# Kernel tuning notes

Hardware: AMD Instinct MI355X
Metric: run time of the kernel (lower is better)

The kernel has to match this reference:

```python
import jax, jax.numpy as jnp
import numpy as np

# Problem sizes
N, D, B = 4096, 2048, 64  # nodes, feature dim, sequential samples
# LARFDSSOM hyperparameters (from __init__ defaults)
A_T = 0.3          # activation threshold
DSBETA = 1e-4      # moving-average rate
E_B = 0.5          # winner learning rate
E_N = 0.01 * E_B   # neighbor learning rate (e_n is multiplied by e_b in __init__)
EPS_DS = 0.01      # relevance smoothing


def setup_inputs() -> dict:
    key = jax.random.key(0)
    k0, k1, k2, k3, k4 = jax.random.split(key, 5)
    return {
        "x": jax.random.uniform(k0, (B, D), jnp.float32),
        "weights": jax.random.uniform(k1, (N, D), jnp.float32),
        "moving_avg": jax.random.uniform(k2, (N, D), jnp.float32),
        "relevances": jax.random.uniform(k3, (N, D), jnp.float32),
        "wins": jnp.zeros((N,), jnp.float32),
        "neighbors": jax.random.randint(k4, (N, N), 0, 2) > 0,
    }


def _som_steps(x, weights, moving_avg, relevances, wins, neighbors):
    """Sequential LARFDSSOM update_map over B samples (codebook at max size,
    so the add_node branch is structurally impossible and the per-sample step
    is either 'update winner + neighbors' or a no-op)."""
    node_ids = jnp.arange(weights.shape[0])

    def step(state, w):
        W, M, R, wn = state
        diff = w[None, :] - W                          # [N, D]
        # weighted_distance + activation
        dists = jnp.sum(R * diff * diff, axis=1)       # [N]
        rel_sum = jnp.sum(R, axis=1)                   # [N]
        act = rel_sum / (rel_sum + dists + 1e-7)
        winner = jnp.argmax(act)
        do_upd = act[winner] >= A_T                    # else no-op (codebook full)
        is_winner = node_ids == winner
        is_nb = neighbors[winner] & (~is_winner)
        # per-node learning rate: e_b for winner, e_n for neighbors, 0 otherwise
        lr = jnp.where(is_winner, E_B, jnp.where(is_nb, E_N, 0.0))[:, None]  # [N, 1]
        # update_node (vectorized over all nodes, masked below)
        dist_abs = jnp.abs(diff)
        M_new = lr * DSBETA * dist_abs + (1.0 - lr * DSBETA) * M
        mx = jnp.max(M_new, axis=1, keepdims=True)
        mn = jnp.min(M_new, axis=1, keepdims=True)
        av = jnp.mean(M_new, axis=1, keepdims=True)
        denom = EPS_DS * (mx - mn)
        # denom == 0 -> original produces NaN then sets relevance to 1.0
        arg = jnp.clip((M_new - av) / jnp.where(denom == 0.0, 1.0, denom), -80.0, 80.0)
        R_new = jnp.where(denom == 0.0, 1.0, 1.0 / (1.0 + jnp.exp(arg)))
        W_new = W + lr * diff
        m = (do_upd & (lr[:, 0] > 0.0))[:, None]       # rows actually touched
        W = jnp.where(m, W_new, W)
        M = jnp.where(m, M_new, M)
        R = jnp.where(m, R_new, R)
        wn = wn + jnp.where(is_winner & do_upd, 1.0, 0.0)
        return (W, M, R, wn), None

    (W, M, R, wn), _ = jax.lax.scan(step, (weights, moving_avg, relevances, wins), x)
    return W


def reference(x, weights, moving_avg, relevances, wins, neighbors):
    return _som_steps(x, weights, moving_avg, relevances, wins, neighbors)
```

## Files before the change

kernel.cpp:

```cpp
#include <hip/hip_runtime.h>
#include <cstddef>

#define NN 4096
#define DD 2048
#define BB 64

constexpr float kAT     = 0.3f;
constexpr float kDSBETA = 1e-4f;
constexpr float kEB     = 0.5f;
constexpr float kEN     = 0.005f;
constexpr float kEPS    = 0.01f;

__device__ __forceinline__ float wave_sum_f(float v) {
#pragma unroll
    for (int o = 32; o; o >>= 1) v += __shfl_xor(v, o, 64);
    return v;
}
__device__ __forceinline__ double wave_sum_d(double v) {
#pragma unroll
    for (int o = 32; o; o >>= 1) v += __shfl_xor(v, o, 64);
    return v;
}
__device__ __forceinline__ float wave_max_f(float v) {
#pragma unroll
    for (int o = 32; o; o >>= 1) v = fmaxf(v, __shfl_xor(v, o, 64));
    return v;
}
__device__ __forceinline__ float wave_min_f(float v) {
#pragma unroll
    for (int o = 32; o; o >>= 1) v = fminf(v, __shfl_xor(v, o, 64));
    return v;
}
__device__ __forceinline__ unsigned long long wave_max_u64(unsigned long long v) {
#pragma unroll
    for (int o = 32; o; o >>= 1) {
        const unsigned long long u = __shfl_xor(v, o, 64);
        v = (u > v) ? u : v;
    }
    return v;
}

__global__ void detect_nb(const unsigned char* __restrict__ nb, unsigned* __restrict__ flag) {
    unsigned v = 0;
    const int i0 = threadIdx.x * 256;
    for (int i = 0; i < 256; i++) {
        const int idx = i0 + i;
        if ((idx & 3) != 0) v |= nb[idx];
    }
    if (v != 0) atomicOr(flag, 1u);
}

__global__ __launch_bounds__(256) void som_step(
    const float* __restrict__ x_upd,
    const float* __restrict__ x_act,
    float* __restrict__ W,
    float* __restrict__ M,
    float* __restrict__ R,
    const void* __restrict__ nb,
    const unsigned* __restrict__ flag,
    const unsigned long long* __restrict__ part_upd,
    unsigned long long* __restrict__ part_act,
    const int stride)
{
    const int n   = blockIdx.x;
    const int tid = threadIdx.x;
    __shared__ float  sred[3][4];
    __shared__ double sredd[2][4];

    float lr = 0.0f;
    if (part_upd != nullptr) {
        unsigned long long k = part_upd[(size_t)(tid & 63) * stride];
        k = wave_max_u64(k);
        const double act_w = __longlong_as_double((long long)(k & ~0xFFFULL));
        const int winner   = 4095 - (int)(k & 0xFFFULL);
        if (act_w >= (double)kAT) {
            if (n == winner) {
                lr = kEB;
            } else {
                const size_t off = (size_t)winner * NN + n;
                const bool isnb = (*flag != 0)
                    ? (((const unsigned char*)nb)[off] != 0)
                    : (((const int*)nb)[off] != 0);
                if (isnb) lr = kEN;
            }
        }
    }
    const bool next = (x_act != nullptr);
    if (lr == 0.0f && !next) return;

    const size_t rowoff = (size_t)n * DD + (size_t)tid * 8;
    const size_t xoff   = (size_t)tid * 8;
    float w[8], r[8];
    *(float4*)(w)     = *(const float4*)(W + rowoff);
    *(float4*)(w + 4) = *(const float4*)(W + rowoff + 4);

    if (lr != 0.0f) {
        float m[8], xu[8], mnew[8];
        *(float4*)(m)      = *(const float4*)(M + rowoff);
        *(float4*)(m + 4)  = *(const float4*)(M + rowoff + 4);
        *(float4*)(xu)     = *(const float4*)(x_upd + xoff);
        *(float4*)(xu + 4) = *(const float4*)(x_upd + xoff + 4);

        const float c1 = lr * kDSBETA;
        const float c2 = 1.0f - c1;
        float psum = 0.0f, pmx = -INFINITY, pmn = INFINITY;
#pragma unroll
        for (int j = 0; j < 8; j++) {
            const float d = xu[j] - w[j];
            w[j] = w[j] + lr * d;
            const float mv = c1 * fabsf(d) + c2 * m[j];
            mnew[j] = mv;
            psum += mv;
            pmx = fmaxf(pmx, mv);
            pmn = fminf(pmn, mv);
        }
        psum = wave_sum_f(psum); pmx = wave_max_f(pmx); pmn = wave_min_f(pmn);
        const int wid = tid >> 6, lane = tid & 63;
        if (lane == 0) { sred[0][wid] = psum; sred[1][wid] = pmx; sred[2][wid] = pmn; }
        __syncthreads();
        const float ts  = sred[0][0] + sred[0][1] + sred[0][2] + sred[0][3];
        const float tmx = fmaxf(fmaxf(sred[1][0], sred[1][1]), fmaxf(sred[1][2], sred[1][3]));
        const float tmn = fminf(fminf(sred[2][0], sred[2][1]), fminf(sred[2][2], sred[2][3]));
        __syncthreads();

        const float av    = ts * (1.0f / (float)DD);
        const float denom = kEPS * (tmx - tmn);
        if (denom == 0.0f) {
#pragma unroll
            for (int j = 0; j < 8; j++) r[j] = 1.0f;
        } else {
#pragma unroll
            for (int j = 0; j < 8; j++) {
                float a = (mnew[j] - av) / denom;
                a = fminf(fmaxf(a, -80.0f), 80.0f);
                r[j] = 1.0f / (1.0f + expf(a));
            }
        }
        *(float4*)(W + rowoff)     = *(float4*)(w);
        *(float4*)(W + rowoff + 4) = *(float4*)(w + 4);
        *(float4*)(M + rowoff)     = *(float4*)(mnew);
        *(float4*)(M + rowoff + 4) = *(float4*)(mnew + 4);
        *(float4*)(R + rowoff)     = *(float4*)(r);
        *(float4*)(R + rowoff + 4) = *(float4*)(r + 4);
    } else {
        *(float4*)(r)     = *(const float4*)(R + rowoff);
        *(float4*)(r + 4) = *(const float4*)(R + rowoff + 4);
    }

    if (next) {
        float xn[8];
        *(float4*)(xn)     = *(const float4*)(x_act + xoff);
        *(float4*)(xn + 4) = *(const float4*)(x_act + xoff + 4);
        double pd = 0.0, ps = 0.0;
#pragma unroll
        for (int j = 0; j < 8; j++) {
            const double d  = (double)xn[j] - (double)w[j];
            const double rj = (double)r[j];
            pd += rj * d * d;
            ps += rj;
        }
        pd = wave_sum_d(pd); ps = wave_sum_d(ps);
        const int wid = tid >> 6, lane = tid & 63;
        if (lane == 0) { sredd[0][wid] = pd; sredd[1][wid] = ps; }
        __syncthreads();
        if (tid == 0) {
            const double td = sredd[0][0] + sredd[0][1] + sredd[0][2] + sredd[0][3];
            const double tr = sredd[1][0] + sredd[1][1] + sredd[1][2] + sredd[1][3];
            const double act = tr / (tr + td + 1e-7);
            const unsigned long long ab = (unsigned long long)__double_as_longlong(act);
            const unsigned long long kk = (ab & ~0xFFFULL) | (unsigned long long)(4095 - n);
            atomicMax(&part_act[(size_t)(n & 63) * stride], kk);
        }
    }
}

extern "C" void kernel_launch(void* const* d_in, const int* in_sizes, int n_in,
                              void* d_out, int out_size, void* d_ws, size_t ws_size,
                              hipStream_t stream) {
    const float* x  = (const float*)d_in[0];
    const float* W0 = (const float*)d_in[1];
    float*       M  = (float*)d_in[2];
    float*       R  = (float*)d_in[3];
    const void*  nb = d_in[5];
    float*       W  = (float*)d_out;

    const int stride = (ws_size >= (size_t)(66 * 64 * 8 * 8 + 64)) ? 8 : 1;
    unsigned long long* part = (unsigned long long*)d_ws;
    const size_t part_bytes = (size_t)65 * 64 * stride * 8;
    unsigned* flagp = (unsigned*)((char*)d_ws + part_bytes);

    hipMemcpyAsync(W, W0, sizeof(float) * (size_t)NN * DD, hipMemcpyDeviceToDevice, stream);
    hipMemsetAsync(d_ws, 0, part_bytes + 64, stream);
    detect_nb<<<1, 256, 0, stream>>>((const unsigned char*)nb, flagp);

    som_step<<<NN, 256, 0, stream>>>(nullptr, x, W, M, R, nb, flagp,
                                     nullptr, part, stride);

    for (int t = 0; t < BB; t++) {
        const float* xu = x + (size_t)t * DD;
        const float* xa = (t < BB - 1) ? (x + (size_t)(t + 1) * DD) : nullptr;
        const unsigned long long* pu = part + (size_t)t * 64 * stride;
        unsigned long long*       pa = (t < BB - 1) ? (part + (size_t)(t + 1) * 64 * stride) : nullptr;
        som_step<<<NN, 256, 0, stream>>>(xu, xa, W, M, R, nb, flagp, pu, pa, stride);
    }
}
```

Measured before the change: 1.695 ms.

## Fuse all SOM steps into one cooperative persistent kernel keeping rows in registers

Replaces the 65 per-step kernel launches with a single cooperative kernel in which each block owns 8 codebook rows and keeps W, M and R for them in registers across all 64 samples. A grid-wide sync separates the steps. This removes the per-step global reloads and stores of the full W/M/R state and the launch overhead. It costs heavy register use (192+ floats per thread), needs every block co-resident for the grid sync, and keeps the old multi-launch path as a fallback.

```diff
diff --git a/kernel.cpp b/kernel.cpp
--- a/kernel.cpp
+++ b/kernel.cpp
@@ -1,9 +1,14 @@
 #include <hip/hip_runtime.h>
+#include <hip/hip_cooperative_groups.h>
 #include <cstddef>
+
+namespace cg = cooperative_groups;
 
 #define NN 4096
 #define DD 2048
 #define BB 64
+#define RPB 8
+#define GRID_BLKS (NN / RPB)
 
 constexpr float kAT     = 0.3f;
 constexpr float kDSBETA = 1e-4f;
@@ -50,17 +55,161 @@
     if (v != 0) atomicOr(flag, 1u);
 }
 
+__global__ __launch_bounds__(256, 2) void som_all(
+    const float* __restrict__ x,
+    const float* __restrict__ W0,
+    const float* __restrict__ M0,
+    const float* __restrict__ R0,
+    const unsigned char* __restrict__ nbb,
+    const unsigned* __restrict__ flag,
+    float* __restrict__ Wout,
+    unsigned long long* __restrict__ part)
+{
+    cg::grid_group grid = cg::this_grid();
+    const int tid  = threadIdx.x;
+    const int wid  = tid >> 6;
+    const int lane = tid & 63;
+    const int n0   = (int)blockIdx.x * RPB;
+    const int col  = tid * 8;
+
+    __shared__ double sdd[2][RPB][4];
+    __shared__ float  sf[3][4];
+    __shared__ unsigned long long skk[RPB];
+
+    const bool nb_byte = (*flag != 0);
+    const int* nbi = (const int*)nbb;
+
+    float w[RPB][8], r[RPB][8], m[RPB][8], xcur[8];
+
+#pragma unroll
+    for (int row = 0; row < RPB; ++row) {
+        const size_t base = (size_t)(n0 + row) * DD + col;
+        *(float4*)(&w[row][0]) = *(const float4*)(W0 + base);
+        *(float4*)(&w[row][4]) = *(const float4*)(W0 + base + 4);
+        *(float4*)(&r[row][0]) = *(const float4*)(R0 + base);
+        *(float4*)(&r[row][4]) = *(const float4*)(R0 + base + 4);
+        *(float4*)(&m[row][0]) = *(const float4*)(M0 + base);
+        *(float4*)(&m[row][4]) = *(const float4*)(M0 + base + 4);
+    }
+    *(float4*)(xcur)     = *(const float4*)(x + col);
+    *(float4*)(xcur + 4) = *(const float4*)(x + col + 4);
+
+    auto act_phase = [&](int slot) {
+#pragma unroll
+        for (int row = 0; row < RPB; ++row) {
+            double pd = 0.0, ps = 0.0;
+#pragma unroll
+            for (int j = 0; j < 8; ++j) {
+                const double d  = (double)xcur[j] - (double)w[row][j];
+                const double rj = (double)r[row][j];
+                pd += rj * d * d;
+                ps += rj;
+            }
+            pd = wave_sum_d(pd); ps = wave_sum_d(ps);
+            if (lane == 0) { sdd[0][row][wid] = pd; sdd[1][row][wid] = ps; }
+        }
+        __syncthreads();
+        if (tid < RPB) {
+            const int row = tid;
+            const double td = sdd[0][row][0] + sdd[0][row][1] + sdd[0][row][2] + sdd[0][row][3];
+            const double tr = sdd[1][row][0] + sdd[1][row][1] + sdd[1][row][2] + sdd[1][row][3];
+            const double act = tr / (tr + td + 1e-7);
+            const unsigned long long ab = (unsigned long long)__double_as_longlong(act);
+            skk[row] = (ab & ~0xFFFULL) | (unsigned long long)(4095 - (n0 + row));
+        }
+        __syncthreads();
+        if (tid == 0) {
+            unsigned long long k = skk[0];
+#pragma unroll
+            for (int i = 1; i < RPB; ++i) k = (skk[i] > k) ? skk[i] : k;
+            atomicMax(&part[(size_t)slot * 64 * 8 + (size_t)(blockIdx.x & 63) * 8], k);
+        }
+    };
+
+    act_phase(0);
+
+    for (int t = 0; t < BB; ++t) {
+        grid.sync();
+
+        unsigned long long k = __hip_atomic_load(
+            &part[(size_t)t * 64 * 8 + (size_t)lane * 8],
+            __ATOMIC_RELAXED, __HIP_MEMORY_SCOPE_AGENT);
+        k = wave_max_u64(k);
+        const double act_w = __longlong_as_double((long long)(k & ~0xFFFULL));
+        const int winner   = 4095 - (int)(k & 0xFFFULL);
+
+        if (act_w >= (double)kAT) {
+#pragma unroll
+            for (int row = 0; row < RPB; ++row) {
+                const int n = n0 + row;
+                float lr = 0.0f;
+                if (n == winner) {
+                    lr = kEB;
+                } else {
+                    const size_t off = (size_t)winner * NN + n;
+                    const bool isnb = nb_byte ? (nbb[off] != 0) : (nbi[off] != 0);
+                    if (isnb) lr = kEN;
+                }
+                if (lr != 0.0f) {
+                    const float c1 = lr * kDSBETA;
+                    const float c2 = 1.0f - c1;
+                    float psum = 0.0f, pmx = -INFINITY, pmn = INFINITY;
+#pragma unroll
+                    for (int j = 0; j < 8; ++j) {
+                        const float d  = xcur[j] - w[row][j];
+                        const float mv = c1 * fabsf(d) + c2 * m[row][j];
+                        w[row][j] += lr * d;
+                        m[row][j] = mv;
+                        psum += mv;
+                        pmx = fmaxf(pmx, mv);
+                        pmn = fminf(pmn, mv);
+                    }
+                    psum = wave_sum_f(psum); pmx = wave_max_f(pmx); pmn = wave_min_f(pmn);
+                    if (lane == 0) { sf[0][wid] = psum; sf[1][wid] = pmx; sf[2][wid] = pmn; }
+                    __syncthreads();
+                    const float ts  = sf[0][0] + sf[0][1] + sf[0][2] + sf[0][3];
+                    const float tmx = fmaxf(fmaxf(sf[1][0], sf[1][1]), fmaxf(sf[1][2], sf[1][3]));
+                    const float tmn = fminf(fminf(sf[2][0], sf[2][1]), fminf(sf[2][2], sf[2][3]));
+                    __syncthreads();
+                    const float av    = ts * (1.0f / (float)DD);
+                    const float denom = kEPS * (tmx - tmn);
+                    if (denom == 0.0f) {
+#pragma unroll
+                        for (int j = 0; j < 8; ++j) r[row][j] = 1.0f;
+                    } else {
+#pragma unroll
+                        for (int j = 0; j < 8; ++j) {
+                            float a = (m[row][j] - av) / denom;
+                            a = fminf(fmaxf(a, -80.0f), 80.0f);
+                            r[row][j] = 1.0f / (1.0f + expf(a));
+                        }
+                    }
+                }
+            }
+        }
+
+        if (t < BB - 1) {
+            const size_t xb = (size_t)(t + 1) * DD + col;
+            *(float4*)(xcur)     = *(const float4*)(x + xb);
+            *(float4*)(xcur + 4) = *(const float4*)(x + xb + 4);
+            act_phase(t + 1);
+        }
+    }
+
+#pragma unroll
+    for (int row = 0; row < RPB; ++row) {
+        const size_t base = (size_t)(n0 + row) * DD + col;
+        *(float4*)(Wout + base)     = *(float4*)(&w[row][0]);
+        *(float4*)(Wout + base + 4) = *(float4*)(&w[row][4]);
+    }
+}
+
 __global__ __launch_bounds__(256) void som_step(
-    const float* __restrict__ x_upd,
-    const float* __restrict__ x_act,
-    float* __restrict__ W,
-    float* __restrict__ M,
-    float* __restrict__ R,
-    const void* __restrict__ nb,
-    const unsigned* __restrict__ flag,
+    const float* __restrict__ x_upd, const float* __restrict__ x_act,
+    float* __restrict__ W, float* __restrict__ M, float* __restrict__ R,
+    const void* __restrict__ nb, const unsigned* __restrict__ flag,
     const unsigned long long* __restrict__ part_upd,
-    unsigned long long* __restrict__ part_act,
-    const int stride)
+    unsigned long long* __restrict__ part_act)
 {
     const int n   = blockIdx.x;
     const int tid = threadIdx.x;
@@ -69,14 +218,13 @@
 
     float lr = 0.0f;
     if (part_upd != nullptr) {
-        unsigned long long k = part_upd[(size_t)(tid & 63) * stride];
+        unsigned long long k = part_upd[(size_t)(tid & 63) * 8];
         k = wave_max_u64(k);
         const double act_w = __longlong_as_double((long long)(k & ~0xFFFULL));
         const int winner   = 4095 - (int)(k & 0xFFFULL);
         if (act_w >= (double)kAT) {
-            if (n == winner) {
-                lr = kEB;
-            } else {
+            if (n == winner) lr = kEB;
+            else {
                 const size_t off = (size_t)winner * NN + n;
                 const bool isnb = (*flag != 0)
                     ? (((const unsigned char*)nb)[off] != 0)
@@ -100,19 +248,15 @@
         *(float4*)(m + 4)  = *(const float4*)(M + rowoff + 4);
         *(float4*)(xu)     = *(const float4*)(x_upd + xoff);
         *(float4*)(xu + 4) = *(const float4*)(x_upd + xoff + 4);
-
-        const float c1 = lr * kDSBETA;
-        const float c2 = 1.0f - c1;
+        const float c1 = lr * kDSBETA, c2 = 1.0f - c1;
         float psum = 0.0f, pmx = -INFINITY, pmn = INFINITY;
 #pragma unroll
         for (int j = 0; j < 8; j++) {
             const float d = xu[j] - w[j];
-            w[j] = w[j] + lr * d;
+            w[j] += lr * d;
             const float mv = c1 * fabsf(d) + c2 * m[j];
-            mnew[j] = mv;
-            psum += mv;
-            pmx = fmaxf(pmx, mv);
-            pmn = fminf(pmn, mv);
+            mnew[j] = mv; psum += mv;
+            pmx = fmaxf(pmx, mv); pmn = fminf(pmn, mv);
         }
         psum = wave_sum_f(psum); pmx = wave_max_f(pmx); pmn = wave_min_f(pmn);
         const int wid = tid >> 6, lane = tid & 63;
@@ -122,8 +266,7 @@
         const float tmx = fmaxf(fmaxf(sred[1][0], sred[1][1]), fmaxf(sred[1][2], sred[1][3]));
         const float tmn = fminf(fminf(sred[2][0], sred[2][1]), fminf(sred[2][2], sred[2][3]));
         __syncthreads();
-
-        const float av    = ts * (1.0f / (float)DD);
+        const float av = ts * (1.0f / (float)DD);
         const float denom = kEPS * (tmx - tmn);
         if (denom == 0.0f) {
 #pragma unroll
@@ -156,8 +299,7 @@
         for (int j = 0; j < 8; j++) {
             const double d  = (double)xn[j] - (double)w[j];
             const double rj = (double)r[j];
-            pd += rj * d * d;
-            ps += rj;
+            pd += rj * d * d; ps += rj;
         }
         pd = wave_sum_d(pd); ps = wave_sum_d(ps);
         const int wid = tid >> 6, lane = tid & 63;
@@ -169,7 +311,7 @@
             const double act = tr / (tr + td + 1e-7);
             const unsigned long long ab = (unsigned long long)__double_as_longlong(act);
             const unsigned long long kk = (ab & ~0xFFFULL) | (unsigned long long)(4095 - n);
-            atomicMax(&part_act[(size_t)(n & 63) * stride], kk);
+            atomicMax(&part_act[(size_t)(n & 63) * 8], kk);
         }
     }
 }
@@ -177,30 +319,43 @@
 extern "C" void kernel_launch(void* const* d_in, const int* in_sizes, int n_in,
                               void* d_out, int out_size, void* d_ws, size_t ws_size,
                               hipStream_t stream) {
-    const float* x  = (const float*)d_in[0];
-    const float* W0 = (const float*)d_in[1];
-    float*       M  = (float*)d_in[2];
-    float*       R  = (float*)d_in[3];
-    const void*  nb = d_in[5];
-    float*       W  = (float*)d_out;
-
-    const int stride = (ws_size >= (size_t)(66 * 64 * 8 * 8 + 64)) ? 8 : 1;
+    const float*         x   = (const float*)d_in[0];
+    const float*         W0  = (const float*)d_in[1];
+    float*               M   = (float*)d_in[2];
+    float*               R   = (float*)d_in[3];
+    const unsigned char* nbb = (const unsigned char*)d_in[5];
+    float*               W   = (float*)d_out;
+
     unsigned long long* part = (unsigned long long*)d_ws;
-    const size_t part_bytes = (size_t)65 * 64 * stride * 8;
-    unsigned* flagp = (unsigned*)((char*)d_ws + part_bytes);
+    const size_t part_bytes  = (size_t)66 * 64 * 8 * sizeof(unsigned long long);
+    unsigned*           flagp = (unsigned*)((char*)d_ws + part_bytes);
+
+    hipMemsetAsync(d_ws, 0, part_bytes + 64, stream);
+    detect_nb<<<1, 256, 0, stream>>>(nbb, flagp);
+
+    int occ = 0;
+    hipError_t qerr = hipOccupancyMaxActiveBlocksPerMultiprocessor(
+        &occ, (const void*)som_all, 256, 0);
+    bool coop_ok = (qerr == hipSuccess && occ >= 2);
+
+    if (coop_ok) {
+        const float* xp = x; const float* w0p = W0; const float* m0p = (const float*)M;
+        const float* r0p = (const float*)R; const unsigned char* nbp = nbb;
+        const unsigned* fp = flagp; float* wp = W; unsigned long long* pp = part;
+        void* args[] = { &xp, &w0p, &m0p, &r0p, &nbp, &fp, &wp, &pp };
+        hipError_t lerr = hipLaunchCooperativeKernel((const void*)som_all,
+                                                     dim3(GRID_BLKS), dim3(256),
+                                                     args, 0, stream);
+        if (lerr == hipSuccess) return;
+    }
 
     hipMemcpyAsync(W, W0, sizeof(float) * (size_t)NN * DD, hipMemcpyDeviceToDevice, stream);
-    hipMemsetAsync(d_ws, 0, part_bytes + 64, stream);
-    detect_nb<<<1, 256, 0, stream>>>((const unsigned char*)nb, flagp);
-
-    som_step<<<NN, 256, 0, stream>>>(nullptr, x, W, M, R, nb, flagp,
-                                     nullptr, part, stride);
-
+    som_step<<<NN, 256, 0, stream>>>(nullptr, x, W, M, R, nbb, flagp, nullptr, part);
     for (int t = 0; t < BB; t++) {
         const float* xu = x + (size_t)t * DD;
         const float* xa = (t < BB - 1) ? (x + (size_t)(t + 1) * DD) : nullptr;
-        const unsigned long long* pu = part + (size_t)t * 64 * stride;
-        unsigned long long*       pa = (t < BB - 1) ? (part + (size_t)(t + 1) * 64 * stride) : nullptr;
-        som_step<<<NN, 256, 0, stream>>>(xu, xa, W, M, R, nb, flagp, pu, pa, stride);
-    }
-}
+        const unsigned long long* pu = part + (size_t)t * 64 * 8;
+        unsigned long long*       pa = (t < BB - 1) ? (part + (size_t)(t + 1) * 64 * 8) : nullptr;
+        som_step<<<NN, 256, 0, stream>>>(xu, xa, W, M, R, nbb, flagp, pu, pa);
+    }
+}
```

After: 1.662 ms. No clear change (-1.9%).
